# Kernel optimization log

Hardware: AMD Instinct MI355X
Metric: run time of the kernel (lower is better)

The kernel has to match this reference:

```python
import jax, jax.numpy as jnp
import numpy as np
from jax import lax

B, C_IN, C_HID, NUM_CLASSES, HW = 128, 256, 1024, 1, 17
DN = ('NCHW', 'OIHW', 'NCHW')


def setup_inputs() -> dict:
    key = jax.random.key(0)
    k = jax.random.split(key, 5)
    x = jax.random.normal(k[0], (B, C_IN, HW, HW), dtype=jnp.float32)
    # ConvRnn stand-in: 3x3 SAME conv 256->1024 + tanh (zero initial hidden state)
    w_rnn = jax.random.normal(k[1], (C_HID, C_IN, 3, 3), dtype=jnp.float32) * 0.02
    b_rnn = jax.random.normal(k[2], (C_HID,), dtype=jnp.float32) * 0.02
    # 1x1 conv 1024 -> NUM_CLASSES
    w_out = jax.random.normal(k[3], (NUM_CLASSES, C_HID, 1, 1), dtype=jnp.float32) * 0.02
    b_out = jax.random.normal(k[4], (NUM_CLASSES,), dtype=jnp.float32) * 0.02
    return {"x": x, "w_rnn": w_rnn, "b_rnn": b_rnn, "w_out": w_out, "b_out": b_out}


def _branch(x, w_rnn, b_rnn, w_out, b_out):
    h = jnp.tanh(
        lax.conv_general_dilated(x, w_rnn, (1, 1), 'SAME', dimension_numbers=DN)
        + b_rnn[None, :, None, None]
    )
    h = jax.nn.relu(h)
    s = lax.conv_general_dilated(h, w_out, (1, 1), 'SAME', dimension_numbers=DN)
    return jax.nn.sigmoid(s + b_out[None, :, None, None])  # [B, NUM_CLASSES, 17, 17]


def reference(x, w_rnn, b_rnn, w_out, b_out):
    score = _branch(x, w_rnn, b_rnn, w_out, b_out)
    # per-sample peak of channel-0 map; first occurrence in row-major order
    flat = score[:, 0].reshape(score.shape[0], -1)          # [B, H*W]
    idx = jnp.argmax(flat, axis=-1)                          # first max, like nonzero()[0]
    pos_list = jnp.stack([idx // HW, idx % HW], axis=-1).astype(jnp.int32)  # [B, 2] = (y, x)
    return (score, pos_list)
```

## Files before the change

### kernel.cpp

```cpp
#include <hip/hip_runtime.h>
#include <hip/hip_bf16.h>

#define HW_ 17
#define P_ 289
#define BIMG 128
#define CIN 256
#define CHID 1024

#define WS_S_OFF    1024
#define WS_W2_OFF   262144
#define WS_X2_OFF   9699328

typedef __attribute__((ext_vector_type(8))) short short8;
typedef __attribute__((ext_vector_type(4))) float float4_t;

#define BHALO_OFF  0
#define BHALO_ROWS 384
#define ABUF_OFF   49152
#define ABUF_SZ    16384
#define LDS_TOTAL  81920

__device__ __forceinline__ unsigned short f32_to_bf16_rne(float f) {
  unsigned int u = __builtin_bit_cast(unsigned int, f);
  unsigned int r = (u + 0x7FFFu + ((u >> 16) & 1u)) >> 16;
  return (unsigned short)r;
}
__device__ __forceinline__ float bf16_bits_to_f32(unsigned short h) {
  unsigned int u = ((unsigned int)h) << 16;
  return __builtin_bit_cast(float, u);
}
__device__ __forceinline__ void glds16(const void* g, void* l) {
  __builtin_amdgcn_global_load_lds(
      (const __attribute__((address_space(1))) void*)g,
      (__attribute__((address_space(3))) void*)l, 16, 0, 0);
}

__global__ void prep_w_kernel(const float* __restrict__ w_rnn,
                              unsigned short* __restrict__ w2) {
  int t = blockIdx.x * 256 + threadIdx.x;
  int c = t & 255;
  int oc = (t >> 8) & 1023;
  int kyx = t >> 18;
  float w = w_rnn[(size_t)(oc * 256 + c) * 9 + kyx];
  unsigned short hi = f32_to_bf16_rne(w);
  unsigned short lo = f32_to_bf16_rne(w - bf16_bits_to_f32(hi));
  size_t base = (size_t)(kyx * 1024 + oc) * 512;
  w2[base + c] = hi;
  w2[base + 256 + c] = lo;
}

__global__ void prep_x_kernel(const float* __restrict__ x,
                              unsigned short* __restrict__ x2) {
  __shared__ unsigned short hibuf[P_ * 34];
  __shared__ unsigned short lobuf[P_ * 34];
  int n = blockIdx.y;
  int c0 = blockIdx.x * 32;
  int t = threadIdx.x;
  for (int ci = 0; ci < 32; ++ci) {
    const float* src = x + (size_t)(n * CIN + c0 + ci) * P_;
    for (int pb = 0; pb < 2; ++pb) {
      int p = pb * 256 + t;
      if (p < P_) {
        float v = src[p];
        unsigned short h = f32_to_bf16_rne(v);
        hibuf[p * 34 + ci] = h;
        lobuf[p * 34 + ci] = f32_to_bf16_rne(v - bf16_bits_to_f32(h));
      }
    }
  }
  __syncthreads();
  int ci = t & 31;
  int psub = t >> 5;
  for (int pb = 0; pb < P_; pb += 8) {
    int p = pb + psub;
    if (p < P_) {
      size_t ob = ((size_t)n * P_ + p) * 512;
      x2[ob + c0 + ci]       = hibuf[p * 34 + ci];
      x2[ob + 256 + c0 + ci] = lobuf[p * 34 + ci];
    }
  }
}

__global__ __launch_bounds__(256, 2) void conv_kernel(
    const unsigned short* __restrict__ w2,
    const unsigned short* __restrict__ x2,
    const float* __restrict__ b_rnn,
    const float* __restrict__ w_out,
    const char* __restrict__ zpage,
    float* __restrict__ sbuf) {
  extern __shared__ char lds[];
  const int t = threadIdx.x;
  const int n = blockIdx.y;
  const int oc0 = blockIdx.x * 128;

  const int lane = t & 63;
  const int wid = t >> 6;
  const int wm = wid >> 1, wn = wid & 1;
  const int lrow = lane & 15, g = lane >> 4;

  const int cc = t & 7;
  const int rr = t >> 3;
  const int sw = cc ^ (rr & 7);

  const char* w2c = (const char*)w2;
  const char* x2c = (const char*)x2;
  const size_t aLaneBase = (size_t)(oc0 + rr) * 1024 + sw * 16;
  char* aDst = lds + ABUF_OFF + (t & ~63) * 16;
  char* bDst = lds + BHALO_OFF + (t & ~63) * 16;

  int pBase[12];
#pragma unroll
  for (int i = 0; i < 12; ++i) {
    int h = i * 32 + rr;
    int hy = h / 19, hx = h - hy * 19;
    bool interior = (h < 361) && (hy >= 1) && (hy <= 17) && (hx >= 1) && (hx <= 17);
    int p = (hy - 1) * 17 + (hx - 1);
    pBase[i] = interior ? (int)((size_t)(n * P_ + p) * 1024 + sw * 16) : -1;
  }

  int aoff[4][2];
#pragma unroll
  for (int i = 0; i < 4; ++i) {
    int row = wm * 64 + i * 16 + lrow;
#pragma unroll
    for (int kk = 0; kk < 2; ++kk)
      aoff[i][kk] = ABUF_OFF + row * 128 + ((kk * 64 + g * 16) ^ ((row & 7) << 4));
  }
  int hb[10];
#pragma unroll
  for (int j = 0; j < 10; ++j) {
    int p = wn * 160 + j * 16 + lrow;
    int py = p / 17;
    hb[j] = (p < P_) ? py * 19 + (p - py * 17) : 0;
  }

  float4_t acc[4][10];
#pragma unroll
  for (int i = 0; i < 4; ++i)
#pragma unroll
    for (int j = 0; j < 10; ++j) acc[i][j] = (float4_t){0.f, 0.f, 0.f, 0.f};

  {
    const char* src = w2c + aLaneBase;
#pragma unroll
    for (int i = 0; i < 4; ++i) glds16(src + i * 32768, aDst + i * 4096);
  }

  for (int s = 0; s < 108; ++s) {
    int seg, rep, tap;
    if (s < 72) { seg = s / 18; int r = s - seg * 18; rep = r / 9; tap = r - rep * 9; }
    else        { int q = s - 72; seg = 4 + q / 9; rep = 0; tap = q - (seg - 4) * 9; }

    if (rep == 0 && tap == 0) {
#pragma unroll
      for (int i = 0; i < 12; ++i) {
        const char* src = (pBase[i] >= 0) ? x2c + pBase[i] + seg * 128 : zpage;
        glds16(src, bDst + i * 4096);
      }
    }
    if (s < 107) {
      int s1 = s + 1, seg1, rep1, tap1;
      if (s1 < 72) { seg1 = s1 / 18; int r = s1 - seg1 * 18; rep1 = r / 9; tap1 = r - rep1 * 9; }
      else         { int q = s1 - 72; seg1 = 4 + q / 9; rep1 = 0; tap1 = q - (seg1 - 4) * 9; }
      int aChunk1 = (seg1 < 4) ? (rep1 ? 4 + seg1 : seg1) : (seg1 - 4);
      const char* src = w2c + aLaneBase + (size_t)tap1 * 1048576 + aChunk1 * 128;
      char* dst = aDst + ((s1 & 1) ? ABUF_SZ : 0);
#pragma unroll
      for (int i = 0; i < 4; ++i) glds16(src + i * 32768, dst + i * 4096);
      asm volatile("s_waitcnt vmcnt(4)" ::: "memory");
    } else {
      asm volatile("s_waitcnt vmcnt(0)" ::: "memory");
    }
    __builtin_amdgcn_s_barrier();

    const int d = (tap / 3) * 19 + (tap - (tap / 3) * 3);
    const int abase = (s & 1) ? ABUF_SZ : 0;
    __builtin_amdgcn_s_setprio(1);
#pragma unroll
    for (int kk = 0; kk < 2; ++kk) {
      short8 af[4];
#pragma unroll
      for (int i = 0; i < 4; ++i)
        af[i] = *(const short8*)(lds + abase + aoff[i][kk]);
#pragma unroll
      for (int jh = 0; jh < 2; ++jh) {
        short8 bf[5];
#pragma unroll
        for (int j5 = 0; j5 < 5; ++j5) {
          int h = hb[jh * 5 + j5] + d;
          int boff = h * 128 + ((kk * 64 + g * 16) ^ ((h & 7) << 4));
          bf[j5] = *(const short8*)(lds + boff);
        }
#pragma unroll
        for (int i = 0; i < 4; ++i)
#pragma unroll
          for (int j5 = 0; j5 < 5; ++j5)
            acc[i][jh * 5 + j5] = __builtin_amdgcn_mfma_f32_16x16x32_bf16(
                af[i], bf[j5], acc[i][jh * 5 + j5], 0, 0, 0);
      }
    }
    __builtin_amdgcn_s_setprio(0);
    __builtin_amdgcn_s_barrier();
    asm volatile("" ::: "memory");
  }

  float sacc[10] = {0.f, 0.f, 0.f, 0.f, 0.f, 0.f, 0.f, 0.f, 0.f, 0.f};
#pragma unroll
  for (int i = 0; i < 4; ++i) {
#pragma unroll
    for (int r = 0; r < 4; ++r) {
      int oc = oc0 + wm * 64 + i * 16 + g * 4 + r;
      float wo = w_out[oc];
      float br = b_rnn[oc];
#pragma unroll
      for (int j = 0; j < 10; ++j) {
        float v = acc[i][j][r] + br;
        float h = tanhf(v);
        h = fmaxf(h, 0.f);
        sacc[j] = fmaf(wo, h, sacc[j]);
      }
    }
  }
#pragma unroll
  for (int j = 0; j < 10; ++j) {
    sacc[j] += __shfl_xor(sacc[j], 16);
    sacc[j] += __shfl_xor(sacc[j], 32);
  }
  if (lane < 16) {
#pragma unroll
    for (int j = 0; j < 10; ++j) {
      int pos = wn * 160 + j * 16 + lrow;
      if (pos < P_) atomicAdd(&sbuf[n * P_ + pos], sacc[j]);
    }
  }
}

__global__ void finalize_kernel(const float* __restrict__ sbuf,
                                const float* __restrict__ b_out,
                                float* __restrict__ out) {
  int n = blockIdx.x;
  int lane = threadIdx.x;
  float bo = b_out[0];
  float vmax = -1e30f;
  int imax = 0x7FFFFFFF;
  for (int p = lane; p < P_; p += 64) {
    float v = sbuf[n * P_ + p] + bo;
    float sg = 1.0f / (1.0f + expf(-v));
    out[n * P_ + p] = sg;
    if (sg > vmax) { vmax = sg; imax = p; }
  }
  for (int off = 32; off >= 1; off >>= 1) {
    float ov = __shfl_xor(vmax, off);
    int oi = __shfl_xor(imax, off);
    if (ov > vmax || (ov == vmax && oi < imax)) { vmax = ov; imax = oi; }
  }
  if (lane == 0) {
    int y = imax / 17;
    int xq = imax - y * 17;
    out[BIMG * P_ + n * 2 + 0] = (float)y;
    out[BIMG * P_ + n * 2 + 1] = (float)xq;
  }
}

extern "C" void kernel_launch(void* const* d_in, const int* in_sizes, int n_in,
                              void* d_out, int out_size, void* d_ws, size_t ws_size,
                              hipStream_t stream) {
  const float* x     = (const float*)d_in[0];
  const float* w_rnn = (const float*)d_in[1];
  const float* b_rnn = (const float*)d_in[2];
  const float* w_out = (const float*)d_in[3];
  const float* b_out = (const float*)d_in[4];
  char* ws = (char*)d_ws;
  unsigned short* w2 = (unsigned short*)(ws + WS_W2_OFF);
  unsigned short* x2 = (unsigned short*)(ws + WS_X2_OFF);
  float* sbuf = (float*)(ws + WS_S_OFF);
  float* out = (float*)d_out;

  hipFuncSetAttribute((const void*)conv_kernel,
                      hipFuncAttributeMaxDynamicSharedMemorySize, LDS_TOTAL);

  hipMemsetAsync(ws, 0, WS_S_OFF + BIMG * P_ * 4, stream);
  prep_w_kernel<<<9216, 256, 0, stream>>>(w_rnn, w2);
  prep_x_kernel<<<dim3(8, 128), 256, 0, stream>>>(x, x2);
  conv_kernel<<<dim3(8, 128), 256, LDS_TOTAL, stream>>>(w2, x2, b_rnn, w_out, ws, sbuf);
  finalize_kernel<<<128, 64, 0, stream>>>(sbuf, b_out, out);
}
```

Baseline: 611.6 us.

## Read conv weights directly from global memory instead of staging through LDS

The A-operand (weights) LDS double buffer is removed. Each wave now loads its weight fragments straight from global memory per tap, and LDS holds only the input halo tile in a static 48KB buffer. The halo swizzle is changed to a (hy+hx)-based XOR pattern with precomputed per-column offsets, so fewer barriers are needed (two per segment instead of two per step). The cost is exposed global-load latency for the weights inside the MFMA loop with no prefetch, traded for lower LDS use and possibly higher occupancy.

```diff
diff --git a/kernel.cpp b/kernel.cpp
--- a/kernel.cpp
+++ b/kernel.cpp
@@ -13,12 +13,6 @@
 
 typedef __attribute__((ext_vector_type(8))) short short8;
 typedef __attribute__((ext_vector_type(4))) float float4_t;
-
-#define BHALO_OFF  0
-#define BHALO_ROWS 384
-#define ABUF_OFF   49152
-#define ABUF_SZ    16384
-#define LDS_TOTAL  81920
 
 __device__ __forceinline__ unsigned short f32_to_bf16_rne(float f) {
   unsigned int u = __builtin_bit_cast(unsigned int, f);
@@ -88,7 +82,7 @@
     const float* __restrict__ w_out,
     const char* __restrict__ zpage,
     float* __restrict__ sbuf) {
-  extern __shared__ char lds[];
+  __shared__ char lds[49152];
   const int t = threadIdx.x;
   const int n = blockIdx.y;
   const int oc0 = blockIdx.x * 128;
@@ -100,39 +94,39 @@
 
   const int cc = t & 7;
   const int rr = t >> 3;
-  const int sw = cc ^ (rr & 7);
-
-  const char* w2c = (const char*)w2;
   const char* x2c = (const char*)x2;
-  const size_t aLaneBase = (size_t)(oc0 + rr) * 1024 + sw * 16;
-  char* aDst = lds + ABUF_OFF + (t & ~63) * 16;
-  char* bDst = lds + BHALO_OFF + (t & ~63) * 16;
-
-  int pBase[12];
+  int pOff[12];
 #pragma unroll
   for (int i = 0; i < 12; ++i) {
     int h = i * 32 + rr;
     int hy = h / 19, hx = h - hy * 19;
+    int f = (hy + hx) & 7;
+    int sw = cc ^ f;
     bool interior = (h < 361) && (hy >= 1) && (hy <= 17) && (hx >= 1) && (hx <= 17);
     int p = (hy - 1) * 17 + (hx - 1);
-    pBase[i] = interior ? (int)((size_t)(n * P_ + p) * 1024 + sw * 16) : -1;
-  }
-
-  int aoff[4][2];
-#pragma unroll
-  for (int i = 0; i < 4; ++i) {
-    int row = wm * 64 + i * 16 + lrow;
-#pragma unroll
-    for (int kk = 0; kk < 2; ++kk)
-      aoff[i][kk] = ABUF_OFF + row * 128 + ((kk * 64 + g * 16) ^ ((row & 7) << 4));
-  }
-  int hb[10];
+    pOff[i] = interior ? (int)(((size_t)(n * P_ + p)) * 1024 + sw * 16) : -1;
+  }
+
+  const char* w2b = (const char*)w2 + (size_t)oc0 * 1024;
+  int avoff[4];
+#pragma unroll
+  for (int i = 0; i < 4; ++i)
+    avoff[i] = (wm * 64 + i * 16 + lrow) * 1024 + g * 16;
+
+  int hb128[10], fbs[10];
 #pragma unroll
   for (int j = 0; j < 10; ++j) {
     int p = wn * 160 + j * 16 + lrow;
-    int py = p / 17;
-    hb[j] = (p < P_) ? py * 19 + (p - py * 17) : 0;
-  }
+    if (p < P_) {
+      int py = p / 17, px = p - py * 17;
+      hb128[j] = (py * 19 + px) * 128;
+      fbs[j] = (py + px) & 7;
+    } else {
+      hb128[j] = 0;
+      fbs[j] = 0;
+    }
+  }
+  const int Cg = g * 16;
 
   float4_t acc[4][10];
 #pragma unroll
@@ -140,68 +134,60 @@
 #pragma unroll
     for (int j = 0; j < 10; ++j) acc[i][j] = (float4_t){0.f, 0.f, 0.f, 0.f};
 
-  {
-    const char* src = w2c + aLaneBase;
-#pragma unroll
-    for (int i = 0; i < 4; ++i) glds16(src + i * 32768, aDst + i * 4096);
-  }
-
-  for (int s = 0; s < 108; ++s) {
-    int seg, rep, tap;
-    if (s < 72) { seg = s / 18; int r = s - seg * 18; rep = r / 9; tap = r - rep * 9; }
-    else        { int q = s - 72; seg = 4 + q / 9; rep = 0; tap = q - (seg - 4) * 9; }
-
-    if (rep == 0 && tap == 0) {
-#pragma unroll
-      for (int i = 0; i < 12; ++i) {
-        const char* src = (pBase[i] >= 0) ? x2c + pBase[i] + seg * 128 : zpage;
-        glds16(src, bDst + i * 4096);
-      }
-    }
-    if (s < 107) {
-      int s1 = s + 1, seg1, rep1, tap1;
-      if (s1 < 72) { seg1 = s1 / 18; int r = s1 - seg1 * 18; rep1 = r / 9; tap1 = r - rep1 * 9; }
-      else         { int q = s1 - 72; seg1 = 4 + q / 9; rep1 = 0; tap1 = q - (seg1 - 4) * 9; }
-      int aChunk1 = (seg1 < 4) ? (rep1 ? 4 + seg1 : seg1) : (seg1 - 4);
-      const char* src = w2c + aLaneBase + (size_t)tap1 * 1048576 + aChunk1 * 128;
-      char* dst = aDst + ((s1 & 1) ? ABUF_SZ : 0);
-#pragma unroll
-      for (int i = 0; i < 4; ++i) glds16(src + i * 32768, dst + i * 4096);
-      asm volatile("s_waitcnt vmcnt(4)" ::: "memory");
-    } else {
-      asm volatile("s_waitcnt vmcnt(0)" ::: "memory");
-    }
-    __builtin_amdgcn_s_barrier();
-
-    const int d = (tap / 3) * 19 + (tap - (tap / 3) * 3);
-    const int abase = (s & 1) ? ABUF_SZ : 0;
+  auto step = [&](int tap, const char* aBase) {
+    short8 af[4][2];
+#pragma unroll
+    for (int i = 0; i < 4; ++i)
+#pragma unroll
+      for (int kk = 0; kk < 2; ++kk)
+        af[i][kk] = *(const short8*)(aBase + avoff[i] + kk * 64);
+    const int dy = tap / 3, dx = tap - 3 * (tap / 3);
+    const int d128 = (dy * 19 + dx) * 128;
+    const int fd = dy + dx;
+    int ba[10];
+#pragma unroll
+    for (int j = 0; j < 10; ++j)
+      ba[j] = hb128[j] + d128 + (Cg ^ (((fbs[j] + fd) & 7) << 4));
     __builtin_amdgcn_s_setprio(1);
 #pragma unroll
     for (int kk = 0; kk < 2; ++kk) {
-      short8 af[4];
-#pragma unroll
-      for (int i = 0; i < 4; ++i)
-        af[i] = *(const short8*)(lds + abase + aoff[i][kk]);
 #pragma unroll
       for (int jh = 0; jh < 2; ++jh) {
         short8 bf[5];
 #pragma unroll
-        for (int j5 = 0; j5 < 5; ++j5) {
-          int h = hb[jh * 5 + j5] + d;
-          int boff = h * 128 + ((kk * 64 + g * 16) ^ ((h & 7) << 4));
-          bf[j5] = *(const short8*)(lds + boff);
-        }
+        for (int j5 = 0; j5 < 5; ++j5)
+          bf[j5] = *(const short8*)(lds + (ba[jh * 5 + j5] ^ (kk * 64)));
 #pragma unroll
         for (int i = 0; i < 4; ++i)
 #pragma unroll
           for (int j5 = 0; j5 < 5; ++j5)
             acc[i][jh * 5 + j5] = __builtin_amdgcn_mfma_f32_16x16x32_bf16(
-                af[i], bf[j5], acc[i][jh * 5 + j5], 0, 0, 0);
+                af[i][kk], bf[j5], acc[i][jh * 5 + j5], 0, 0, 0);
       }
     }
     __builtin_amdgcn_s_setprio(0);
-    __builtin_amdgcn_s_barrier();
-    asm volatile("" ::: "memory");
+  };
+
+  for (int seg = 0; seg < 8; ++seg) {
+    __syncthreads();
+#pragma unroll
+    for (int i = 0; i < 12; ++i) {
+      const char* src = (pOff[i] >= 0) ? x2c + (size_t)pOff[i] + seg * 128 : zpage;
+      glds16(src, lds + wid * 1024 + i * 4096);
+    }
+    __syncthreads();
+    if (seg < 4) {
+#pragma unroll
+      for (int tap = 0; tap < 9; ++tap)
+        step(tap, w2b + (size_t)tap * 1048576 + seg * 128);
+#pragma unroll
+      for (int tap = 0; tap < 9; ++tap)
+        step(tap, w2b + (size_t)tap * 1048576 + seg * 128 + 512);
+    } else {
+#pragma unroll
+      for (int tap = 0; tap < 9; ++tap)
+        step(tap, w2b + (size_t)tap * 1048576 + (seg - 4) * 128);
+    }
   }
 
   float sacc[10] = {0.f, 0.f, 0.f, 0.f, 0.f, 0.f, 0.f, 0.f, 0.f, 0.f};
@@ -276,12 +262,9 @@
   float* sbuf = (float*)(ws + WS_S_OFF);
   float* out = (float*)d_out;
 
-  hipFuncSetAttribute((const void*)conv_kernel,
-                      hipFuncAttributeMaxDynamicSharedMemorySize, LDS_TOTAL);
-
   hipMemsetAsync(ws, 0, WS_S_OFF + BIMG * P_ * 4, stream);
   prep_w_kernel<<<9216, 256, 0, stream>>>(w_rnn, w2);
   prep_x_kernel<<<dim3(8, 128), 256, 0, stream>>>(x, x2);
-  conv_kernel<<<dim3(8, 128), 256, LDS_TOTAL, stream>>>(w2, x2, b_rnn, w_out, ws, sbuf);
+  conv_kernel<<<dim3(8, 128), 256, 0, stream>>>(w2, x2, b_rnn, w_out, ws, sbuf);
   finalize_kernel<<<128, 64, 0, stream>>>(sbuf, b_out, out);
 }
```

Result: slower. 1.673 ms (+173.6%).
